# Optimization experiments

Measured on AMD Instinct MI355X. Metric: run time of the kernel, lower is better.

## Reference

```python
import jax, jax.numpy as jnp
import numpy as np

H = 8       # heads
D = 512     # hidden_size
DH = D // H # head dim
FF = 2048   # hardcoded FFN hidden in source


def _layernorm(x, g, b, eps=1e-5):
    mu = jnp.mean(x, axis=-1, keepdims=True)
    var = jnp.var(x, axis=-1, keepdims=True)
    return (x - mu) * jax.lax.rsqrt(var + eps) * g + b


def setup_inputs() -> dict:
    key = jax.random.key(0)
    ks = jax.random.split(key, 12)
    B, S = 2, 4096
    s = lambda fan_in: 1.0 / np.sqrt(fan_in)
    return {
        "reaction": jax.random.normal(ks[0], (B, S, D), dtype=jnp.float32),
        "mask": jnp.ones((B, 1, 1, S), dtype=jnp.int32),
        # attention weights stored as [in, out] (torch Linear weight.T)
        "Wq": jax.random.uniform(ks[1], (D, D), jnp.float32, -s(D), s(D)),
        "Wk": jax.random.uniform(ks[2], (D, D), jnp.float32, -s(D), s(D)),
        "Wv": jax.random.uniform(ks[3], (D, D), jnp.float32, -s(D), s(D)),
        "Wo": jax.random.uniform(ks[4], (D, D), jnp.float32, -s(D), s(D)),
        "bo": jnp.zeros((D,), jnp.float32),
        "W1": jax.random.uniform(ks[5], (D, FF), jnp.float32, -s(D), s(D)),
        "b1": jnp.zeros((FF,), jnp.float32),
        "W2": jax.random.uniform(ks[6], (FF, D), jnp.float32, -s(FF), s(FF)),
        "b2": jnp.zeros((D,), jnp.float32),
        "g_sa": jnp.ones((D,), jnp.float32),
        "b_sa": jnp.zeros((D,), jnp.float32),
        "g_ff": jnp.ones((D,), jnp.float32),
        "b_ff": jnp.zeros((D,), jnp.float32),
    }


def reference(reaction, mask, Wq, Wk, Wv, Wo, bo, W1, b1, W2, b2, g_sa, b_sa, g_ff, b_ff):
    B, S, _ = reaction.shape
    # --- self-attention part (pre-norm) ---
    x = _layernorm(reaction, g_sa, b_sa)
    q = (x @ Wq).reshape(B, S, H, DH)
    k = (x @ Wk).reshape(B, S, H, DH)
    v = (x @ Wv).reshape(B, S, H, DH)
    scale = DH ** (-0.5)
    scores = jnp.einsum('bqhd,bkhd->bhqk', q * scale, k)  # [B,H,S,S]
    scores = jnp.where(mask == 0, -jnp.inf, scores)
    att = jax.nn.softmax(scores, axis=-1)
    ctx = jnp.einsum('bhqk,bkhd->bqhd', att, v).reshape(B, S, D)
    attn_out = jax.nn.gelu(ctx @ Wo + bo, approximate=False)  # GELU after output proj (as in source)
    x = attn_out + reaction
    # --- feed-forward part (pre-norm) ---
    y = _layernorm(x, g_ff, b_ff)
    y = jax.nn.gelu(y @ W1 + b1, approximate=False) @ W2 + b2
    return y + x
```

## Files before the change

kernel.cpp:

```cpp
#include <hip/hip_runtime.h>
#include <hip/hip_bf16.h>
#include <math.h>

#define HN 8
#define DM 512
#define DHD 64
#define FFD 2048
#define BB 2
#define SS 4096
#define MT (BB*SS)

typedef __bf16 bf16_t;
typedef __bf16 bf16x8 __attribute__((ext_vector_type(8)));
typedef __bf16 bf16x4 __attribute__((ext_vector_type(4)));
typedef float  floatx4 __attribute__((ext_vector_type(4)));

__device__ __forceinline__ void async_copy16(const bf16_t* g, bf16_t* l) {
  __builtin_amdgcn_global_load_lds((const __attribute__((address_space(1))) void*)g,
                                   (__attribute__((address_space(3))) void*)l,
                                   16, 0, 0);
}

#if __has_builtin(__builtin_amdgcn_exp2f)
__device__ __forceinline__ float fast_exp2(float x) { return __builtin_amdgcn_exp2f(x); }
#else
__device__ __forceinline__ float fast_exp2(float x) { return __expf(x * 0.69314718056f); }
#endif

__device__ __forceinline__ float gelu_f(float x) {
  float y = 0.7978845608f * (x + 0.044715f * x * x * x);
  float e = fast_exp2(y * 2.885390082f);
  float th = 1.0f - 2.0f / (e + 1.0f);
  return 0.5f * x * (1.0f + th);
}

__global__ __launch_bounds__(256)
void ln_kernel(const float* __restrict__ x, const float* __restrict__ g,
               const float* __restrict__ be, bf16_t* __restrict__ out)
{
  const int wave = threadIdx.x >> 6, lane = threadIdx.x & 63;
  const int row = blockIdx.x * 4 + wave;
  const float* xr = x + (size_t)row * DM + lane * 8;
  float4 a = *(const float4*)xr;
  float4 c = *(const float4*)(xr + 4);
  float s  = (a.x + a.y) + (a.z + a.w) + (c.x + c.y) + (c.z + c.w);
  float s2 = (a.x*a.x + a.y*a.y) + (a.z*a.z + a.w*a.w)
           + (c.x*c.x + c.y*c.y) + (c.z*c.z + c.w*c.w);
#pragma unroll
  for (int o = 1; o < 64; o <<= 1) { s += __shfl_xor(s, o); s2 += __shfl_xor(s2, o); }
  const float mu = s * (1.0f / DM);
  const float rv = rsqrtf(s2 * (1.0f / DM) - mu * mu + 1e-5f);
  float4 g0 = *(const float4*)(g + lane * 8);
  float4 g1 = *(const float4*)(g + lane * 8 + 4);
  float4 b0 = *(const float4*)(be + lane * 8);
  float4 b1 = *(const float4*)(be + lane * 8 + 4);
  bf16x8 o8;
  o8[0] = (bf16_t)((a.x - mu) * rv * g0.x + b0.x);
  o8[1] = (bf16_t)((a.y - mu) * rv * g0.y + b0.y);
  o8[2] = (bf16_t)((a.z - mu) * rv * g0.z + b0.z);
  o8[3] = (bf16_t)((a.w - mu) * rv * g0.w + b0.w);
  o8[4] = (bf16_t)((c.x - mu) * rv * g1.x + b1.x);
  o8[5] = (bf16_t)((c.y - mu) * rv * g1.y + b1.y);
  o8[6] = (bf16_t)((c.z - mu) * rv * g1.z + b1.z);
  o8[7] = (bf16_t)((c.w - mu) * rv * g1.w + b1.w);
  *(bf16x8*)(out + (size_t)row * DM + lane * 8) = o8;
}

__global__ __launch_bounds__(256)
void prep_weights(const float* __restrict__ Wq, const float* __restrict__ Wk,
                  const float* __restrict__ Wv, const float* __restrict__ Wo,
                  const float* __restrict__ W1, const float* __restrict__ W2,
                  bf16_t* __restrict__ WqkvT, bf16_t* __restrict__ WoT,
                  bf16_t* __restrict__ W1T, bf16_t* __restrict__ W2T)
{
  const int bid = blockIdx.x;
  const float* src; bf16_t* dst; int Kd, Nd, n0, k0;
  if (bid < 768) {
    int seg = bid >> 8, t = bid & 255;
    src = (seg == 0) ? Wq : (seg == 1) ? Wk : Wv;
    dst = WqkvT + (size_t)seg * 512 * 512;
    Kd = 512; Nd = 512; n0 = (t & 15) * 32; k0 = (t >> 4) * 32;
  } else if (bid < 1024) {
    int t = bid - 768; src = Wo; dst = WoT;
    Kd = 512; Nd = 512; n0 = (t & 15) * 32; k0 = (t >> 4) * 32;
  } else if (bid < 2048) {
    int t = bid - 1024; src = W1; dst = W1T;
    Kd = 512; Nd = 2048; n0 = (t & 63) * 32; k0 = (t >> 6) * 32;
  } else {
    int t = bid - 2048; src = W2; dst = W2T;
    Kd = 2048; Nd = 512; n0 = (t & 15) * 32; k0 = (t >> 4) * 32;
  }
  __shared__ float tile[32][33];
  const int tx = threadIdx.x & 31, ty = threadIdx.x >> 5;
#pragma unroll
  for (int i = 0; i < 32; i += 8)
    tile[ty + i][tx] = src[(size_t)(k0 + ty + i) * Nd + n0 + tx];
  __syncthreads();
#pragma unroll
  for (int i = 0; i < 32; i += 8)
    dst[(size_t)(n0 + ty + i) * Kd + k0 + tx] = (bf16_t)tile[tx][ty + i];
}

template <int MI, int NJ, int EPI>
__global__ __launch_bounds__(256)
void gemm_bt(const bf16_t* __restrict__ A, const bf16_t* __restrict__ Bt,
             const int M, const int N, const int K,
             const float* __restrict__ bias, const float* __restrict__ res,
             bf16_t* __restrict__ outb, float* __restrict__ outf,
             bf16_t* __restrict__ out2, bf16_t* __restrict__ out3, const int ldt)
{
  constexpr int MTILE = 32 * MI, NTILE = 32 * NJ;
  constexpr int ACOPY = MTILE / 32;
  constexpr int BCOPY = NTILE / 32;
  __shared__ __align__(16) bf16_t lA[MTILE * 64];
  __shared__ __align__(16) bf16_t lB[NTILE * 64];
  const int tid = threadIdx.x;
  const int wave = tid >> 6, lane = tid & 63;
  const int wm = wave & 1, wn = wave >> 1;
  const int quad = lane >> 4, l16 = lane & 15;

  int srA[ACOPY > BCOPY ? ACOPY : BCOPY], scA[ACOPY > BCOPY ? ACOPY : BCOPY];
#pragma unroll
  for (int i = 0; i < (ACOPY > BCOPY ? ACOPY : BCOPY); ++i) {
    int flat = tid + 256 * i;
    int r = flat >> 3, ch = flat & 7;
    srA[i] = r;
    scA[i] = (ch ^ (r & 7)) * 8;
  }
  const bf16_t* Ab = A + (size_t)(blockIdx.x * MTILE) * K;
  const bf16_t* Bb = Bt + (size_t)(blockIdx.y * NTILE) * K;

  const floatx4 vzero = {0.f, 0.f, 0.f, 0.f};
  floatx4 acc[MI][NJ];
#pragma unroll
  for (int i = 0; i < MI; ++i)
#pragma unroll
    for (int j = 0; j < NJ; ++j) acc[i][j] = vzero;

  for (int k0 = 0; k0 < K; k0 += 64) {
    __syncthreads();
#pragma unroll
    for (int i = 0; i < ACOPY; ++i)
      async_copy16(Ab + (size_t)srA[i] * K + k0 + scA[i], lA + (tid + 256 * i) * 8);
#pragma unroll
    for (int i = 0; i < BCOPY; ++i)
      async_copy16(Bb + (size_t)srA[i] * K + k0 + scA[i], lB + (tid + 256 * i) * 8);
    __syncthreads();
#pragma unroll
    for (int c = 0; c < 2; ++c) {
      bf16x8 af[MI], bfv[NJ];
#pragma unroll
      for (int i = 0; i < MI; ++i)
        af[i] = *(const bf16x8*)(lA + (wm * 16 * MI + i * 16 + l16) * 64
                                 + (((c * 4 + quad) ^ (l16 & 7)) * 8));
#pragma unroll
      for (int j = 0; j < NJ; ++j)
        bfv[j] = *(const bf16x8*)(lB + (wn * 16 * NJ + j * 16 + l16) * 64
                                  + (((c * 4 + quad) ^ (l16 & 7)) * 8));
#pragma unroll
      for (int i = 0; i < MI; ++i)
#pragma unroll
        for (int j = 0; j < NJ; ++j)
          acc[i][j] = __builtin_amdgcn_mfma_f32_16x16x32_bf16(af[i], bfv[j], acc[i][j], 0, 0, 0);
    }
  }

  const int m00 = blockIdx.x * MTILE + wm * 16 * MI;
  const int n00 = blockIdx.y * NTILE + wn * 16 * NJ;
#pragma unroll
  for (int i = 0; i < MI; ++i) {
#pragma unroll
    for (int j = 0; j < NJ; ++j) {
      const int m0 = m00 + i * 16 + quad * 4;
      const int n  = n00 + j * 16 + l16;
      floatx4 v = acc[i][j];
      if (EPI == 2) {
        const float bb = bias[n];
#pragma unroll
        for (int r = 0; r < 4; ++r)
          outf[(size_t)(m0 + r) * N + n] = gelu_f(v[r] + bb) + res[(size_t)(m0 + r) * N + n];
      } else if (EPI == 3) {
        const float bb = bias[n];
#pragma unroll
        for (int r = 0; r < 4; ++r)
          outb[(size_t)(m0 + r) * N + n] = (bf16_t)gelu_f(v[r] + bb);
      } else if (EPI == 4) {
        const float bb = bias[n];
#pragma unroll
        for (int r = 0; r < 4; ++r)
          outf[(size_t)(m0 + r) * N + n] = v[r] + bb + res[(size_t)(m0 + r) * N + n];
      } else {
        const int seg = blockIdx.y >> 2;
        if (seg == 0) {
#pragma unroll
          for (int r = 0; r < 4; ++r)
            outb[(size_t)(m0 + r) * 512 + n] = (bf16_t)(v[r] * 0.180336879f);
        } else if (seg == 1) {
#pragma unroll
          for (int r = 0; r < 4; ++r) out2[(size_t)(m0 + r) * 512 + (n - 512)] = (bf16_t)v[r];
        } else {
          const int o = m0 & 31;
          const int p0 = (m0 & ~31) + ((o >> 2) & 3) * 8 + ((o >> 4) << 2);
          bf16x4 pk = {(bf16_t)v[0], (bf16_t)v[1], (bf16_t)v[2], (bf16_t)v[3]};
          *(bf16x4*)(out3 + (size_t)(n - 1024) * ldt + p0) = pk;
        }
      }
    }
  }
}

__global__ __launch_bounds__(256, 2)
void attn_kernel(const bf16_t* __restrict__ qm, const bf16_t* __restrict__ km,
                 const bf16_t* __restrict__ vtm, const int* __restrict__ mask,
                 bf16_t* __restrict__ ctx)
{
  const int b = blockIdx.z, h = blockIdx.y;
  const int q0 = blockIdx.x * 128;
  const int tid = threadIdx.x;
  const int wave = tid >> 6, lane = tid & 63;
  const int quad = lane >> 4, l16 = lane & 15;

  __shared__ __align__(16) bf16_t lK[128 * DHD];
  __shared__ __align__(16) bf16_t lV[DHD * 128];
  __shared__ int sclean[4];

  const int* maskb = mask + b * SS;

  unsigned um = 0xFFFFFFFFu;
#pragma unroll
  for (int i = 0; i < 4; ++i) {
    int4 m = *(const int4*)(maskb + tid * 16 + i * 4);
    um = min(um, min(min((unsigned)m.x, (unsigned)m.y), min((unsigned)m.z, (unsigned)m.w)));
  }
#pragma unroll
  for (int o = 1; o < 64; o <<= 1) um = min(um, (unsigned)__shfl_xor((int)um, o));
  if (lane == 0) sclean[wave] = (int)um;
  __syncthreads();
  const bool clean = (min(min((unsigned)sclean[0], (unsigned)sclean[1]),
                          min((unsigned)sclean[2], (unsigned)sclean[3])) != 0u);

  const size_t qrow0 = (size_t)b * SS + q0;
  bf16x8 qa[2][2];
#pragma unroll
  for (int mb = 0; mb < 2; ++mb)
#pragma unroll
    for (int cc = 0; cc < 2; ++cc)
      qa[mb][cc] = *(const bf16x8*)(qm + (qrow0 + wave * 32 + mb * 16 + l16) * DM
                                    + h * DHD + cc * 32 + quad * 8);

  const floatx4 vzero = {0.f, 0.f, 0.f, 0.f};
  floatx4 cacc[2][4];
  float lsum[2] = {0.f, 0.f};
#pragma unroll
  for (int mb = 0; mb < 2; ++mb)
#pragma unroll
    for (int nb = 0; nb < 4; ++nb) cacc[mb][nb] = vzero;

  const bf16_t* Kb = km + (size_t)b * SS * DM + h * DHD;
  const bf16_t* Vb = vtm + (size_t)(h * DHD) * MT + (size_t)b * SS;

  for (int s0 = 0; s0 < SS; s0 += 128) {
    __syncthreads();
#pragma unroll
    for (int i = 0; i < 4; ++i) {
      int p = tid + 256 * i;
      int key = p >> 3;
      int cs = (p & 7) ^ (key & 7);
      async_copy16(Kb + (size_t)(s0 + key) * DM + cs * 8, lK + p * 8);
      int dh = p >> 4;
      int cs2 = (p & 15) ^ (dh & 7);
      async_copy16(Vb + (size_t)dh * MT + s0 + cs2 * 8, lV + p * 8);
    }
    __syncthreads();

#pragma unroll
    for (int c = 0; c < 4; ++c) {
      floatx4 sa[2], sb[2];
      sa[0] = vzero; sa[1] = vzero; sb[0] = vzero; sb[1] = vzero;
#pragma unroll
      for (int cc = 0; cc < 2; ++cc) {
        const int ko = ((cc * 4 + quad) ^ (l16 & 7)) * 8;
        bf16x8 kf0 = *(const bf16x8*)(lK + (c * 32 + l16) * 64 + ko);
        bf16x8 kf1 = *(const bf16x8*)(lK + (c * 32 + 16 + l16) * 64 + ko);
#pragma unroll
        for (int mb = 0; mb < 2; ++mb) {
          sa[mb] = __builtin_amdgcn_mfma_f32_16x16x32_bf16(kf0, qa[mb][cc], sa[mb], 0, 0, 0);
          sb[mb] = __builtin_amdgcn_mfma_f32_16x16x32_bf16(kf1, qa[mb][cc], sb[mb], 0, 0, 0);
        }
      }

      if (!clean) {
        const int4 m0 = *(const int4*)(maskb + s0 + c * 32 + quad * 4);
        const int4 m1 = *(const int4*)(maskb + s0 + c * 32 + 16 + quad * 4);
#pragma unroll
        for (int mb = 0; mb < 2; ++mb) {
          if (m0.x == 0) sa[mb][0] = -1e30f;
          if (m0.y == 0) sa[mb][1] = -1e30f;
          if (m0.z == 0) sa[mb][2] = -1e30f;
          if (m0.w == 0) sa[mb][3] = -1e30f;
          if (m1.x == 0) sb[mb][0] = -1e30f;
          if (m1.y == 0) sb[mb][1] = -1e30f;
          if (m1.z == 0) sb[mb][2] = -1e30f;
          if (m1.w == 0) sb[mb][3] = -1e30f;
        }
      }

      bf16x8 pf[2];
#pragma unroll
      for (int mb = 0; mb < 2; ++mb) {
        float e0 = fast_exp2(sa[mb][0]), e1 = fast_exp2(sa[mb][1]);
        float e2 = fast_exp2(sa[mb][2]), e3 = fast_exp2(sa[mb][3]);
        float e4 = fast_exp2(sb[mb][0]), e5 = fast_exp2(sb[mb][1]);
        float e6 = fast_exp2(sb[mb][2]), e7 = fast_exp2(sb[mb][3]);
        lsum[mb] += ((e0 + e1) + (e2 + e3)) + ((e4 + e5) + (e6 + e7));
        pf[mb][0] = (bf16_t)e0; pf[mb][1] = (bf16_t)e1;
        pf[mb][2] = (bf16_t)e2; pf[mb][3] = (bf16_t)e3;
        pf[mb][4] = (bf16_t)e4; pf[mb][5] = (bf16_t)e5;
        pf[mb][6] = (bf16_t)e6; pf[mb][7] = (bf16_t)e7;
      }
      const int ch = (c * 4 + quad) ^ (l16 & 7);
#pragma unroll
      for (int nb = 0; nb < 4; ++nb) {
        bf16x8 av = *(const bf16x8*)(lV + (nb * 16 + l16) * 128 + ch * 8);
        cacc[0][nb] = __builtin_amdgcn_mfma_f32_16x16x32_bf16(av, pf[0], cacc[0][nb], 0, 0, 0);
        cacc[1][nb] = __builtin_amdgcn_mfma_f32_16x16x32_bf16(av, pf[1], cacc[1][nb], 0, 0, 0);
      }
    }
  }

#pragma unroll
  for (int mb = 0; mb < 2; ++mb) {
    float tot = lsum[mb];
    tot += __shfl_xor(tot, 16);
    tot += __shfl_xor(tot, 32);
    const float inv = 1.0f / tot;
    const size_t qrow = qrow0 + wave * 32 + mb * 16 + l16;
#pragma unroll
    for (int nb = 0; nb < 4; ++nb) {
      bf16x4 o = {(bf16_t)(cacc[mb][nb][0] * inv), (bf16_t)(cacc[mb][nb][1] * inv),
                  (bf16_t)(cacc[mb][nb][2] * inv), (bf16_t)(cacc[mb][nb][3] * inv)};
      *(bf16x4*)(ctx + qrow * DM + h * DHD + nb * 16 + quad * 4) = o;
    }
  }
}

extern "C" void kernel_launch(void* const* d_in, const int* in_sizes, int n_in,
                              void* d_out, int out_size, void* d_ws, size_t ws_size,
                              hipStream_t stream)
{
  (void)in_sizes; (void)n_in; (void)out_size; (void)ws_size;
  const float* reaction = (const float*)d_in[0];
  const int*   mask     = (const int*)d_in[1];
  const float* Wq = (const float*)d_in[2];
  const float* Wk = (const float*)d_in[3];
  const float* Wv = (const float*)d_in[4];
  const float* Wo = (const float*)d_in[5];
  const float* bo = (const float*)d_in[6];
  const float* W1 = (const float*)d_in[7];
  const float* b1 = (const float*)d_in[8];
  const float* W2 = (const float*)d_in[9];
  const float* b2 = (const float*)d_in[10];
  const float* g_sa = (const float*)d_in[11];
  const float* b_sa = (const float*)d_in[12];
  const float* g_ff = (const float*)d_in[13];
  const float* b_ff = (const float*)d_in[14];
  float* out = (float*)d_out;

  char* ws = (char*)d_ws;
  size_t off = 0;
  auto take = [&](size_t bytes) -> char* {
    char* p = ws + off;
    off += (bytes + 255) & ~(size_t)255;
    return p;
  };

  bf16_t* xln   = (bf16_t*)take((size_t)MT * DM * 2);
  bf16_t* WqkvT = (bf16_t*)take((size_t)3 * DM * DM * 2);
  bf16_t* WoT   = (bf16_t*)take((size_t)DM * DM * 2);
  bf16_t* W1T   = (bf16_t*)take((size_t)FFD * DM * 2);
  bf16_t* W2T   = (bf16_t*)take((size_t)DM * FFD * 2);
  bf16_t* qb    = (bf16_t*)take((size_t)MT * DM * 2);
  bf16_t* kb    = (bf16_t*)take((size_t)MT * DM * 2);
  bf16_t* vtb   = (bf16_t*)take((size_t)DM * MT * 2);
  bf16_t* ctx   = (bf16_t*)take((size_t)MT * DM * 2);
  float*  x2    = (float*)take((size_t)MT * DM * 4);
  bf16_t* yb    = xln;
  bf16_t* hb    = qb;

  ln_kernel<<<MT / 4, 256, 0, stream>>>(reaction, g_sa, b_sa, xln);
  prep_weights<<<3072, 256, 0, stream>>>(Wq, Wk, Wv, Wo, W1, W2, WqkvT, WoT, W1T, W2T);

  gemm_bt<4, 4, 5><<<dim3(64, 12), 256, 0, stream>>>(xln, WqkvT, MT, 3 * DM, DM,
                                                     nullptr, nullptr, qb, nullptr, kb, vtb, MT);

  attn_kernel<<<dim3(SS / 128, HN, BB), 256, 0, stream>>>(qb, kb, vtb, mask, ctx);

  gemm_bt<4, 2, 2><<<dim3(64, 8), 256, 0, stream>>>(ctx, WoT, MT, DM, DM,
                                                    bo, reaction, nullptr, x2, nullptr, nullptr, 0);

  ln_kernel<<<MT / 4, 256, 0, stream>>>(x2, g_ff, b_ff, yb);
  gemm_bt<4, 4, 3><<<dim3(64, 16), 256, 0, stream>>>(yb, W1T, MT, FFD, DM,
                                                     b1, nullptr, hb, nullptr, nullptr, nullptr, 0);
  gemm_bt<4, 2, 4><<<dim3(64, 8), 256, 0, stream>>>(hb, W2T, MT, DM, FFD,
                                                    b2, x2, nullptr, out, nullptr, nullptr, 0);
}
```

Baseline: 283.1 us.

## Double-buffer K/V tiles in attention and swizzle blocks for L2 locality

The attention kernel now keeps two LDS buffers for K and V. The next 128-key tile is loaded asynchronously while MFMAs run on the current tile, with one barrier per half-step instead of two serialized barriers around each load. Blocks are remapped so that each XCD processes contiguous query blocks of the same (batch, head), which improves K/V reuse in L2. Per-thread source pointers are precomputed, and s_setprio raises wave priority around the MFMA bursts. The cost is twice the LDS per block (64KB), which could limit occupancy.

After: 271.1 us. -4.2%, faster.

```diff
diff --git a/kernel.cpp b/kernel.cpp
--- a/kernel.cpp
+++ b/kernel.cpp
@@ -214,14 +214,16 @@
                  const bf16_t* __restrict__ vtm, const int* __restrict__ mask,
                  bf16_t* __restrict__ ctx)
 {
-  const int b = blockIdx.z, h = blockIdx.y;
-  const int q0 = blockIdx.x * 128;
+  const int flat = blockIdx.x + 32 * (blockIdx.y + 8 * blockIdx.z);
+  const int swz = (flat & 7) * 64 + (flat >> 3);
+  const int b = swz >> 8, h = (swz >> 5) & 7;
+  const int q0 = (swz & 31) * 128;
   const int tid = threadIdx.x;
   const int wave = tid >> 6, lane = tid & 63;
   const int quad = lane >> 4, l16 = lane & 15;
 
-  __shared__ __align__(16) bf16_t lK[128 * DHD];
-  __shared__ __align__(16) bf16_t lV[DHD * 128];
+  __shared__ __align__(16) bf16_t lK[2][128 * DHD];
+  __shared__ __align__(16) bf16_t lV[2][DHD * 128];
   __shared__ int sclean[4];
 
   const int* maskb = mask + b * SS;
@@ -259,20 +261,27 @@
   const bf16_t* Kb = km + (size_t)b * SS * DM + h * DHD;
   const bf16_t* Vb = vtm + (size_t)(h * DHD) * MT + (size_t)b * SS;
 
-  for (int s0 = 0; s0 < SS; s0 += 128) {
-    __syncthreads();
+  const bf16_t* pk[4]; const bf16_t* pv[4];
+#pragma unroll
+  for (int i = 0; i < 4; ++i) {
+    int p = tid + 256 * i;
+    int key = p >> 3, cs = (p & 7) ^ (key & 7);
+    pk[i] = Kb + (size_t)key * DM + cs * 8;
+    int dh = p >> 4, cs2 = (p & 15) ^ (dh & 7);
+    pv[i] = Vb + (size_t)dh * MT + cs2 * 8;
+  }
+
+  auto stage = [&](int buf, int s0) {
 #pragma unroll
     for (int i = 0; i < 4; ++i) {
-      int p = tid + 256 * i;
-      int key = p >> 3;
-      int cs = (p & 7) ^ (key & 7);
-      async_copy16(Kb + (size_t)(s0 + key) * DM + cs * 8, lK + p * 8);
-      int dh = p >> 4;
-      int cs2 = (p & 15) ^ (dh & 7);
-      async_copy16(Vb + (size_t)dh * MT + s0 + cs2 * 8, lV + p * 8);
+      int p8 = (tid + 256 * i) * 8;
+      async_copy16(pk[i] + (size_t)s0 * DM, lK[buf] + p8);
+      async_copy16(pv[i] + s0, lV[buf] + p8);
     }
-    __syncthreads();
-
+  };
+
+  auto compute = [&](const bf16_t* __restrict__ lKb, const bf16_t* __restrict__ lVb,
+                     int s0) {
 #pragma unroll
     for (int c = 0; c < 4; ++c) {
       floatx4 sa[2], sb[2];
@@ -280,13 +289,15 @@
 #pragma unroll
       for (int cc = 0; cc < 2; ++cc) {
         const int ko = ((cc * 4 + quad) ^ (l16 & 7)) * 8;
-        bf16x8 kf0 = *(const bf16x8*)(lK + (c * 32 + l16) * 64 + ko);
-        bf16x8 kf1 = *(const bf16x8*)(lK + (c * 32 + 16 + l16) * 64 + ko);
+        bf16x8 kf0 = *(const bf16x8*)(lKb + (c * 32 + l16) * 64 + ko);
+        bf16x8 kf1 = *(const bf16x8*)(lKb + (c * 32 + 16 + l16) * 64 + ko);
+        __builtin_amdgcn_s_setprio(1);
 #pragma unroll
         for (int mb = 0; mb < 2; ++mb) {
           sa[mb] = __builtin_amdgcn_mfma_f32_16x16x32_bf16(kf0, qa[mb][cc], sa[mb], 0, 0, 0);
           sb[mb] = __builtin_amdgcn_mfma_f32_16x16x32_bf16(kf1, qa[mb][cc], sb[mb], 0, 0, 0);
         }
+        __builtin_amdgcn_s_setprio(0);
       }
 
       if (!clean) {
@@ -319,13 +330,26 @@
         pf[mb][6] = (bf16_t)e6; pf[mb][7] = (bf16_t)e7;
       }
       const int ch = (c * 4 + quad) ^ (l16 & 7);
+      __builtin_amdgcn_s_setprio(1);
 #pragma unroll
       for (int nb = 0; nb < 4; ++nb) {
-        bf16x8 av = *(const bf16x8*)(lV + (nb * 16 + l16) * 128 + ch * 8);
+        bf16x8 av = *(const bf16x8*)(lVb + (nb * 16 + l16) * 128 + ch * 8);
         cacc[0][nb] = __builtin_amdgcn_mfma_f32_16x16x32_bf16(av, pf[0], cacc[0][nb], 0, 0, 0);
         cacc[1][nb] = __builtin_amdgcn_mfma_f32_16x16x32_bf16(av, pf[1], cacc[1][nb], 0, 0, 0);
       }
+      __builtin_amdgcn_s_setprio(0);
     }
+  };
+
+  stage(0, 0);
+#pragma unroll 1
+  for (int s0 = 0; s0 < SS; s0 += 256) {
+    __syncthreads();
+    stage(1, s0 + 128);
+    compute(lK[0], lV[0], s0);
+    __syncthreads();
+    if (s0 + 256 < SS) stage(0, s0 + 256);
+    compute(lK[1], lV[1], s0 + 128);
   }
 
 #pragma unroll
```
